# Optimization experiments

Hardware: AMD Instinct MI355X
Metric: run time of the kernel (lower is better)

The kernel has to match this reference:

```python
import jax, jax.numpy as jnp
import numpy as np

N = 100000
E = 1600000
D = 128      # input_dim == hidden_dim
C = 40       # output_dim
L = 3        # num_layers
EPS = 1e-12  # F.normalize eps


def setup_inputs() -> dict:
    key = jax.random.key(0)
    ks = jax.random.split(key, 8)
    x = jax.random.normal(ks[0], (N, D), dtype=jnp.float32)
    edge_index = jax.random.randint(ks[1], (2, E), 0, N, dtype=jnp.int64)
    s = 1.0 / np.sqrt(D)
    # SAGEConv: lin_l (neighbor path, with bias), lin_r (root path, no bias)
    Wl = jax.random.uniform(ks[2], (L, D, D), jnp.float32, -s, s)
    bl = jax.random.uniform(ks[3], (L, D), jnp.float32, -s, s)
    Wr = jax.random.uniform(ks[4], (L, D, D), jnp.float32, -s, s)
    Wlin = jax.random.uniform(ks[5], (C, D), jnp.float32, -s, s)
    blin = jax.random.uniform(ks[6], (C,), jnp.float32, -s, s)
    return {"x": x, "edge_index": edge_index, "Wl": Wl, "bl": bl,
            "Wr": Wr, "Wlin": Wlin, "blin": blin}


def reference(x, edge_index, Wl, bl, Wr, Wlin, blin):
    src, dst = edge_index[0], edge_index[1]
    # in-degree counts for mean aggregation (computed once, reused per layer)
    cnt = jax.ops.segment_sum(jnp.ones((E,), jnp.float32), dst, num_segments=N)
    inv_cnt = (1.0 / jnp.maximum(cnt, 1.0))[:, None]  # [N,1]
    z = x
    for i in range(L):
        msg = z[src]  # gather [E, D]
        agg = jax.ops.segment_sum(msg, dst, num_segments=N) * inv_cnt  # mean [N, D]
        out = agg @ Wl[i].T + bl[i] + z @ Wr[i].T
        # SAGEConv normalize=True: L2 normalize per node
        nrm = jnp.linalg.norm(out, axis=-1, keepdims=True)
        out = out / jnp.maximum(nrm, EPS)
        z = jax.nn.relu(out)  # dropout p=0 -> identity
    return z @ Wlin.T + blin  # [N, C]
```

## Files before the change

### kernel.cpp

```cpp
#include <hip/hip_runtime.h>


typedef __bf16 bf16x8 __attribute__((ext_vector_type(8)));
typedef float  f32x4  __attribute__((ext_vector_type(4)));

#define MFMA16(a, b, c) __builtin_amdgcn_mfma_f32_16x16x32_bf16((a), (b), (c), 0, 0, 0)

__device__ __forceinline__ unsigned rne_bf16(float f) {
  unsigned u = __float_as_uint(f);
  unsigned r = u + 0x7FFFu + ((u >> 16) & 1u);
  return r >> 16;
}

__device__ __forceinline__ float bf_lo(unsigned u) { return __uint_as_float(u << 16); }
__device__ __forceinline__ float bf_hi(unsigned u) { return __uint_as_float(u & 0xFFFF0000u); }

__device__ __forceinline__ void gload_lds16(const void* g, void* l) {
  __builtin_amdgcn_global_load_lds(
      (const __attribute__((address_space(1))) unsigned int*)g,
      (__attribute__((address_space(3))) unsigned int*)l, 16, 0, 0);
}

__global__ __launch_bounds__(256) void prep_k(
    const float* __restrict__ x, const float* __restrict__ Wl,
    const float* __restrict__ Wr, const float* __restrict__ Wlin,
    uint2* __restrict__ planeA, unsigned short* __restrict__ wfrag,
    unsigned short* __restrict__ wlf, int* __restrict__ gcur,
    int cap, int n4) {
  const int b = blockIdx.x;
  const int tid = threadIdx.x;
  if (b == 0) {
    if (tid < 128) gcur[tid] = tid * cap;
    return;
  }
  if (b <= 96) {
    int id = (b - 1) * 256 + tid;
    int l = id & 63;
    int c = (id >> 6) & 7;
    int t = (id >> 9) & 7;
    int p = (id >> 12) & 1;
    int layer = id >> 13;
    int col = t * 16 + (l & 15);
    int kbase = c * 32 + (l >> 4) * 8;
    unsigned short* dst = wfrag + (size_t)layer * 65536 +
                          ((((size_t)p * 8 + t) * 8 + c) * 64 + l) * 8;
#pragma unroll
    for (int j = 0; j < 8; ++j) {
      int k = kbase + j;
      float w = (k < 128) ? Wl[layer * 16384 + col * 128 + k]
                          : Wr[layer * 16384 + col * 128 + (k - 128)];
      unsigned h = rne_bf16(w);
      unsigned o;
      if (p == 0) o = h;
      else o = rne_bf16(w - __uint_as_float(h << 16));
      dst[j] = (unsigned short)o;
    }
    return;
  }
  if (b == 97) {
    for (int id = tid; id < 3 * 4 * 64; id += 256) {
      int l = id & 63;
      int c = (id >> 6) & 3;
      int t = id >> 8;
      int col = t * 16 + (l & 15);
      int kbase = c * 32 + (l >> 4) * 8;
      unsigned short* dst = wlf + (size_t)id * 8;
#pragma unroll
      for (int j = 0; j < 8; ++j) {
        float w = (col < 40) ? Wlin[col * 128 + kbase + j] : 0.f;
        dst[j] = (unsigned short)rne_bf16(w);
      }
    }
    return;
  }
  int i = (b - 98) * 256 + tid;
  if (i >= n4) return;
  float4 f = ((const float4*)x)[i];
  uint2 o;
  o.x = rne_bf16(f.x) | (rne_bf16(f.y) << 16);
  o.y = rne_bf16(f.z) | (rne_bf16(f.w) << 16);
  planeA[i] = o;
}


__global__ __launch_bounds__(256) void bucketA_k(
    const int* __restrict__ src, const int* __restrict__ dst,
    int* __restrict__ gcur, unsigned* __restrict__ coarse, int E, int nc) {
  __shared__ int hist[128];
  __shared__ int sd[128];
  __shared__ int lpos[128];
  __shared__ int gbase[128];
  __shared__ unsigned stage[2048];
  __shared__ unsigned char sbuck[2048];

  const int tid = threadIdx.x;
  const int e0 = blockIdx.x * 2048;

  if (tid < 128) hist[tid] = 0;
  __syncthreads();

  int bv[8], pk[8];
#pragma unroll
  for (int j = 0; j < 8; ++j) {
    int e = e0 + j * 256 + tid;
    bv[j] = -1;
    if (e < E) {
      int s = src[e], d = dst[e];
      bv[j] = d >> 10;
      pk[j] = s | ((d & 1023) << 17);
      atomicAdd(&hist[bv[j]], 1);
    }
  }
  __syncthreads();

  if (tid < 128) sd[tid] = hist[tid];
  __syncthreads();
  for (int off = 1; off < 128; off <<= 1) {
    int t = 0;
    if (tid < 128 && tid >= off) t = sd[tid - off];
    __syncthreads();
    if (tid < 128) sd[tid] += t;
    __syncthreads();
  }
  if (tid < 128) {
    int excl = sd[tid] - hist[tid];
    lpos[tid] = excl;
    gbase[tid] = (tid < nc && hist[tid] > 0) ? atomicAdd(&gcur[tid], hist[tid]) : 0;
  }
  __syncthreads();

#pragma unroll
  for (int j = 0; j < 8; ++j) {
    if (bv[j] >= 0) {
      int slot = atomicAdd(&lpos[bv[j]], 1);
      stage[slot] = (unsigned)pk[j];
      sbuck[slot] = (unsigned char)bv[j];
    }
  }
  __syncthreads();

  const int total = sd[127];
  for (int i = tid; i < total; i += 256) {
    int b = sbuck[i];
    int excl = sd[b] - hist[b];
    coarse[gbase[b] + (i - excl)] = stage[i];
  }
}

__global__ __launch_bounds__(256) void bucketB_k(
    const int* __restrict__ gcur, const unsigned* __restrict__ coarse, int cap,
    int* __restrict__ esrc, int* __restrict__ offsets,
    float* __restrict__ inv_cnt, int n, int nc) {
  __shared__ int hcnt[1024];
  __shared__ int cur[1024];
  __shared__ int sd[256];
  __shared__ int sh_gdst;

  const int tid = threadIdx.x;
  const int b = blockIdx.x;
  const int base = b * 1024;
  const int nn = (n - base < 1024) ? (n - base) : 1024;
  const int wbeg = b * cap;
  const int wend = gcur[b];

  if (tid < 128) {
    int v = (tid < nc) ? (gcur[tid] - tid * cap) : 0;
    sd[tid] = v;
  }
  __syncthreads();
  for (int off = 1; off < 128; off <<= 1) {
    int u = 0;
    if (tid < 128 && tid >= off) u = sd[tid - off];
    __syncthreads();
    if (tid < 128) sd[tid] += u;
    __syncthreads();
  }
  if (tid == b) sh_gdst = sd[tid] - (wend - wbeg);
  for (int j = tid; j < 1024; j += 256) hcnt[j] = 0;
  __syncthreads();
  const int gdst = sh_gdst;

  for (int idx = wbeg + tid; idx < wend; idx += 256)
    atomicAdd(&hcnt[coarse[idx] >> 17], 1);
  __syncthreads();

  int b0 = hcnt[tid * 4], b1 = hcnt[tid * 4 + 1];
  int b2 = hcnt[tid * 4 + 2], b3 = hcnt[tid * 4 + 3];
  int tot = b0 + b1 + b2 + b3;
  sd[tid] = tot;
  __syncthreads();
  for (int off = 1; off < 256; off <<= 1) {
    int u = (tid >= off) ? sd[tid - off] : 0;
    __syncthreads();
    sd[tid] += u;
    __syncthreads();
  }
  int excl = gdst + sd[tid] - tot;
  cur[tid * 4]     = excl;
  cur[tid * 4 + 1] = excl + b0;
  cur[tid * 4 + 2] = excl + b0 + b1;
  cur[tid * 4 + 3] = excl + b0 + b1 + b2;
  __syncthreads();

  for (int j = tid; j < nn; j += 256) {
    offsets[base + j] = cur[j];
    int c = hcnt[j] > 1 ? hcnt[j] : 1;
    inv_cnt[base + j] = 1.0f / (float)c;
  }
  if (tid == 0 && base + nn >= n) offsets[n] = gdst + (wend - wbeg);
  __syncthreads();

  for (int idx = wbeg + tid; idx < wend; idx += 256) {
    unsigned p = coarse[idx];
    int pos = atomicAdd(&cur[p >> 17], 1);
    esrc[pos] = (int)(p & 0x1FFFFu);
  }
}

__global__ void aggregate_k(const unsigned short* __restrict__ zb,
                            const int* __restrict__ offsets,
                            const int* __restrict__ esrc,
                            const float* __restrict__ inv_cnt,
                            unsigned short* __restrict__ aggh, int n) {
  int node = (blockIdx.x * 256 + threadIdx.x) >> 4;
  int l16 = threadIdx.x & 15;
  if (node >= n) return;
  int beg = offsets[node], end = offsets[node + 1];
  float a0 = 0.f, a1 = 0.f, a2 = 0.f, a3 = 0.f;
  float a4 = 0.f, a5 = 0.f, a6 = 0.f, a7 = 0.f;
  int t = beg;
  for (; t + 4 <= end; t += 4) {
    int s0 = esrc[t], s1 = esrc[t + 1], s2 = esrc[t + 2], s3 = esrc[t + 3];
    uint4 d0 = *(const uint4*)(zb + (size_t)s0 * 128 + l16 * 8);
    uint4 d1 = *(const uint4*)(zb + (size_t)s1 * 128 + l16 * 8);
    uint4 d2 = *(const uint4*)(zb + (size_t)s2 * 128 + l16 * 8);
    uint4 d3 = *(const uint4*)(zb + (size_t)s3 * 128 + l16 * 8);
    a0 += bf_lo(d0.x); a1 += bf_hi(d0.x); a2 += bf_lo(d0.y); a3 += bf_hi(d0.y);
    a4 += bf_lo(d0.z); a5 += bf_hi(d0.z); a6 += bf_lo(d0.w); a7 += bf_hi(d0.w);
    a0 += bf_lo(d1.x); a1 += bf_hi(d1.x); a2 += bf_lo(d1.y); a3 += bf_hi(d1.y);
    a4 += bf_lo(d1.z); a5 += bf_hi(d1.z); a6 += bf_lo(d1.w); a7 += bf_hi(d1.w);
    a0 += bf_lo(d2.x); a1 += bf_hi(d2.x); a2 += bf_lo(d2.y); a3 += bf_hi(d2.y);
    a4 += bf_lo(d2.z); a5 += bf_hi(d2.z); a6 += bf_lo(d2.w); a7 += bf_hi(d2.w);
    a0 += bf_lo(d3.x); a1 += bf_hi(d3.x); a2 += bf_lo(d3.y); a3 += bf_hi(d3.y);
    a4 += bf_lo(d3.z); a5 += bf_hi(d3.z); a6 += bf_lo(d3.w); a7 += bf_hi(d3.w);
  }
  for (; t + 2 <= end; t += 2) {
    int s0 = esrc[t], s1 = esrc[t + 1];
    uint4 d0 = *(const uint4*)(zb + (size_t)s0 * 128 + l16 * 8);
    uint4 d1 = *(const uint4*)(zb + (size_t)s1 * 128 + l16 * 8);
    a0 += bf_lo(d0.x); a1 += bf_hi(d0.x); a2 += bf_lo(d0.y); a3 += bf_hi(d0.y);
    a4 += bf_lo(d0.z); a5 += bf_hi(d0.z); a6 += bf_lo(d0.w); a7 += bf_hi(d0.w);
    a0 += bf_lo(d1.x); a1 += bf_hi(d1.x); a2 += bf_lo(d1.y); a3 += bf_hi(d1.y);
    a4 += bf_lo(d1.z); a5 += bf_hi(d1.z); a6 += bf_lo(d1.w); a7 += bf_hi(d1.w);
  }
  if (t < end) {
    int s0 = esrc[t];
    uint4 d0 = *(const uint4*)(zb + (size_t)s0 * 128 + l16 * 8);
    a0 += bf_lo(d0.x); a1 += bf_hi(d0.x); a2 += bf_lo(d0.y); a3 += bf_hi(d0.y);
    a4 += bf_lo(d0.z); a5 += bf_hi(d0.z); a6 += bf_lo(d0.w); a7 += bf_hi(d0.w);
  }
  float ic = inv_cnt[node];
  uint4 hv;
  hv.x = rne_bf16(a0 * ic) | (rne_bf16(a1 * ic) << 16);
  hv.y = rne_bf16(a2 * ic) | (rne_bf16(a3 * ic) << 16);
  hv.z = rne_bf16(a4 * ic) | (rne_bf16(a5 * ic) << 16);
  hv.w = rne_bf16(a6 * ic) | (rne_bf16(a7 * ic) << 16);
  *(uint4*)(aggh + (size_t)node * 128 + l16 * 8) = hv;
}

template <bool FUSE>
__global__ __launch_bounds__(256) void sage_layer_mfma_k(
    const unsigned short* __restrict__ zb, const unsigned short* __restrict__ aggh,
    const unsigned short* __restrict__ wf, const float* __restrict__ bl,
    unsigned short* __restrict__ out_bf,
    const unsigned short* __restrict__ wlf, const float* __restrict__ blin,
    float* __restrict__ fout, int n, int ntiles) {
  __shared__ unsigned short Ah_s[32 * 256];
  __shared__ unsigned short Zt_s[FUSE ? 32 * 128 : 8];
  __shared__ float psum[2][4][16];

  const int lane = threadIdx.x & 63;
  const int wv = threadIdx.x >> 6;
  const int g = lane >> 4;
  const int rl = lane & 15;

  const bf16x8* wfv = (const bf16x8*)wf;
  const int t0 = wv * 2, t1 = wv * 2 + 1;
  bf16x8 Bh0[8], Bh1[8], Bl0[8], Bl1[8];
#pragma unroll
  for (int c = 0; c < 8; ++c) {
    Bh0[c] = wfv[((0 * 8 + t0) * 8 + c) * 64 + lane];
    Bh1[c] = wfv[((0 * 8 + t1) * 8 + c) * 64 + lane];
    Bl0[c] = wfv[((1 * 8 + t0) * 8 + c) * 64 + lane];
    Bl1[c] = wfv[((1 * 8 + t1) * 8 + c) * 64 + lane];
  }
  const float b0 = bl[t0 * 16 + rl];
  const float b1 = bl[t1 * 16 + rl];

  char* pAh = (char*)Ah_s;
  char* pZt = (char*)Zt_s;
  const bf16x8* wlfv = (const bf16x8*)wlf;

  const int rsub = lane >> 5;
  const int hlf = (lane >> 4) & 1;
  const int b16 = lane & 15;

  for (int tile = blockIdx.x; tile < ntiles; tile += gridDim.x) {
    const int v0 = tile * 32;

#pragma unroll
    for (int q = 0; q < 4; ++q) {
      int wq = wv * 4 + q;
      int r = wq * 2 + rsub;
      int v = v0 + r; v = (v < n) ? v : (n - 1);
      int sblk = b16 ^ (r & 7);
      const unsigned short* srcp =
          (hlf ? zb : aggh) + (size_t)v * 128 + sblk * 8;
      gload_lds16(srcp, pAh + wq * 1024);
    }
    __syncthreads();

#pragma unroll
    for (int s = 0; s < 2; ++s) {
      f32x4 a0 = {0.f, 0.f, 0.f, 0.f};
      f32x4 a1 = {0.f, 0.f, 0.f, 0.f};
      const int rowH = (s * 16 + rl) * 512;
      const int swz = (rl & 7) << 4;
#pragma unroll
      for (int c = 0; c < 8; ++c) {
        int offH = (rowH + c * 64 + g * 16) ^ swz;
        bf16x8 ah = *(const bf16x8*)(pAh + offH);
        a0 = MFMA16(ah, Bh0[c], a0); a1 = MFMA16(ah, Bh1[c], a1);
        a0 = MFMA16(ah, Bl0[c], a0); a1 = MFMA16(ah, Bl1[c], a1);
      }
      float pr[4];
#pragma unroll
      for (int j = 0; j < 4; ++j) {
        a0[j] += b0; a1[j] += b1;
        pr[j] = a0[j] * a0[j] + a1[j] * a1[j];
      }
#pragma unroll
      for (int m = 1; m < 16; m <<= 1) {
#pragma unroll
        for (int j = 0; j < 4; ++j) pr[j] += __shfl_xor(pr[j], m);
      }
      if (rl == 0) {
#pragma unroll
        for (int j = 0; j < 4; ++j) psum[s][wv][g * 4 + j] = pr[j];
      }
      __syncthreads();
#pragma unroll
      for (int j = 0; j < 4; ++j) {
        int row16 = g * 4 + j;
        float tot = psum[s][0][row16] + psum[s][1][row16] +
                    psum[s][2][row16] + psum[s][3][row16];
        float inv = 1.0f / fmaxf(sqrtf(tot), 1e-12f);
        int v = v0 + s * 16 + row16;
        float o0 = fmaxf(a0[j] * inv, 0.f);
        float o1 = fmaxf(a1[j] * inv, 0.f);
        unsigned short q0 = (unsigned short)rne_bf16(o0);
        unsigned short q1 = (unsigned short)rne_bf16(o1);
        if (!FUSE) {
          if (v < n) {
            out_bf[(size_t)v * 128 + t0 * 16 + rl] = q0;
            out_bf[(size_t)v * 128 + t1 * 16 + rl] = q1;
          }
        } else {
          int rloc = s * 16 + row16;
          int sw = (rloc & 7) << 4;
          *(unsigned short*)(pZt + ((rloc * 256 + (t0 * 16 + rl) * 2) ^ sw)) = q0;
          *(unsigned short*)(pZt + ((rloc * 256 + (t1 * 16 + rl) * 2) ^ sw)) = q1;
        }
      }
    }

    if (FUSE) {
      __syncthreads();
      for (int job = wv; job < 6; job += 4) {
        int s = job / 3, t = job % 3;
        f32x4 acc = {0.f, 0.f, 0.f, 0.f};
        const int rowz = s * 16 + rl;
        const int swzz = (rowz & 7) << 4;
#pragma unroll
        for (int c = 0; c < 4; ++c) {
          bf16x8 a = *(const bf16x8*)(pZt + ((rowz * 256 + c * 64 + g * 16) ^ swzz));
          bf16x8 bw = wlfv[(t * 4 + c) * 64 + lane];
          acc = MFMA16(a, bw, acc);
        }
        int col = t * 16 + rl;
        if (col < 40) {
          float bb = blin[col];
#pragma unroll
          for (int j = 0; j < 4; ++j) {
            int v = v0 + s * 16 + g * 4 + j;
            if (v < n) fout[(size_t)v * 40 + col] = acc[j] + bb;
          }
        }
      }
    }
    __syncthreads();
  }
}


extern "C" void kernel_launch(void* const* d_in, const int* in_sizes, int n_in,
                              void* d_out, int out_size, void* d_ws, size_t ws_size,
                              hipStream_t stream) {
  const float* x    = (const float*)d_in[0];
  const int*   ei   = (const int*)d_in[1];
  const float* Wl   = (const float*)d_in[2];
  const float* bl   = (const float*)d_in[3];
  const float* Wr   = (const float*)d_in[4];
  const float* Wlin = (const float*)d_in[5];
  const float* blin = (const float*)d_in[6];

  const int N = in_sizes[0] / 128;
  const int E = in_sizes[1] / 2;
  const int D = 128;
  const int NC = (N + 1023) >> 10;
  const int cap = (E + NC - 1) / NC + 4096;

  const int* src = ei;
  const int* dstp = ei + E;

  unsigned short* planeA = (unsigned short*)d_ws;
  unsigned short* planeB = planeA + (size_t)N * D;
  unsigned short* aggh   = planeB + (size_t)N * D;
  float* inv_cnt = (float*)(aggh + (size_t)N * D);
  unsigned short* wlf = (unsigned short*)(inv_cnt + N);
  unsigned short* Wfrag = wlf + 6144;
  int*   offsets = (int*)(Wfrag + 3 * 65536);
  int*   esrc    = offsets + N + 1;
  unsigned* coarse = (unsigned*)(esrc + E);
  int*   gcur    = (int*)(coarse + (size_t)NC * cap);

  const int n4 = N * 32;
  prep_k<<<98 + (n4 + 255) / 256, 256, 0, stream>>>(
      x, Wl, Wr, Wlin, (uint2*)planeA, Wfrag, wlf, gcur, cap, n4);

  bucketA_k<<<(E + 2047) / 2048, 256, 0, stream>>>(src, dstp, gcur, coarse, E, NC);
  bucketB_k<<<NC, 256, 0, stream>>>(gcur, coarse, cap, esrc, offsets, inv_cnt, N, NC);

  const int aggGrid = (N * 16 + 255) / 256;
  const int ntiles = (N + 31) / 32;
  const int sageGrid = 1024;

  aggregate_k<<<aggGrid, 256, 0, stream>>>(planeA, offsets, esrc, inv_cnt, aggh, N);
  sage_layer_mfma_k<false><<<sageGrid, 256, 0, stream>>>(
      planeA, aggh, Wfrag + 0 * 65536, bl + 0 * D, planeB, wlf, blin, nullptr, N, ntiles);
  aggregate_k<<<aggGrid, 256, 0, stream>>>(planeB, offsets, esrc, inv_cnt, aggh, N);
  sage_layer_mfma_k<false><<<sageGrid, 256, 0, stream>>>(
      planeB, aggh, Wfrag + 1 * 65536, bl + 1 * D, planeA, wlf, blin, nullptr, N, ntiles);
  aggregate_k<<<aggGrid, 256, 0, stream>>>(planeA, offsets, esrc, inv_cnt, aggh, N);
  sage_layer_mfma_k<true><<<sageGrid, 256, 0, stream>>>(
      planeA, aggh, Wfrag + 2 * 65536, bl + 2 * D, nullptr, wlf, blin,
      (float*)d_out, N, ntiles);
}
```

Measured before the change: 352.5 us.

## Double-buffer SAGE layer tiles in LDS and merge per-subtile norm reductions

The SAGE layer kernel now prefetches the next tile's aggregate and root features into a second LDS buffer with async global-to-LDS loads while the current tile is computed. Both 16-row subtiles are accumulated together before one shared norm reduction, which cuts the number of barriers per tile. The persistent grid shrinks from 1024 to 768 blocks to account for the larger LDS footprint. The aim is to hide global load latency behind MFMA work. The cost is more LDS per block, which may lower occupancy, and barriers that may force the prefetch to finish early.

```diff
diff --git a/kernel.cpp b/kernel.cpp
--- a/kernel.cpp
+++ b/kernel.cpp
@@ -275,9 +275,9 @@
     unsigned short* __restrict__ out_bf,
     const unsigned short* __restrict__ wlf, const float* __restrict__ blin,
     float* __restrict__ fout, int n, int ntiles) {
-  __shared__ unsigned short Ah_s[32 * 256];
+  __shared__ unsigned short Ah_s[2][32 * 256];
   __shared__ unsigned short Zt_s[FUSE ? 32 * 128 : 8];
-  __shared__ float psum[2][4][16];
+  __shared__ float psum[2][2][4][16];
 
   const int lane = threadIdx.x & 63;
   const int wv = threadIdx.x >> 6;
@@ -297,7 +297,6 @@
   const float b0 = bl[t0 * 16 + rl];
   const float b1 = bl[t1 * 16 + rl];
 
-  char* pAh = (char*)Ah_s;
   char* pZt = (char*)Zt_s;
   const bf16x8* wlfv = (const bf16x8*)wlf;
 
@@ -305,59 +304,101 @@
   const int hlf = (lane >> 4) & 1;
   const int b16 = lane & 15;
 
-  for (int tile = blockIdx.x; tile < ntiles; tile += gridDim.x) {
+  int tile = blockIdx.x;
+  if (tile >= ntiles) return;
+
+  {
     const int v0 = tile * 32;
-
 #pragma unroll
     for (int q = 0; q < 4; ++q) {
       int wq = wv * 4 + q;
       int r = wq * 2 + rsub;
       int v = v0 + r; v = (v < n) ? v : (n - 1);
       int sblk = b16 ^ (r & 7);
-      const unsigned short* srcp =
-          (hlf ? zb : aggh) + (size_t)v * 128 + sblk * 8;
-      gload_lds16(srcp, pAh + wq * 1024);
+      gload_lds16((hlf ? zb : aggh) + (size_t)v * 128 + sblk * 8,
+                  (char*)Ah_s[0] + wq * 1024);
+    }
+  }
+  __syncthreads();
+
+  int cur = 0, par = 0;
+  while (tile < ntiles) {
+    const int next = tile + gridDim.x;
+    if (next < ntiles) {
+      const int v0n = next * 32;
+#pragma unroll
+      for (int q = 0; q < 4; ++q) {
+        int wq = wv * 4 + q;
+        int r = wq * 2 + rsub;
+        int v = v0n + r; v = (v < n) ? v : (n - 1);
+        int sblk = b16 ^ (r & 7);
+        gload_lds16((hlf ? zb : aggh) + (size_t)v * 128 + sblk * 8,
+                    (char*)Ah_s[cur ^ 1] + wq * 1024);
+      }
+    }
+
+    const int v0 = tile * 32;
+    char* pAh = (char*)Ah_s[cur];
+
+    f32x4 a00 = {0.f,0.f,0.f,0.f}, a10 = {0.f,0.f,0.f,0.f};
+    f32x4 a01 = {0.f,0.f,0.f,0.f}, a11 = {0.f,0.f,0.f,0.f};
+    {
+      const int swz = (rl & 7) << 4;
+      const int row0 = rl * 512;
+      const int row1 = (16 + rl) * 512;
+#pragma unroll
+      for (int c = 0; c < 8; ++c) {
+        int o0 = (row0 + c * 64 + g * 16) ^ swz;
+        int o1 = (row1 + c * 64 + g * 16) ^ swz;
+        bf16x8 ah0 = *(const bf16x8*)(pAh + o0);
+        bf16x8 ah1 = *(const bf16x8*)(pAh + o1);
+        a00 = MFMA16(ah0, Bh0[c], a00); a10 = MFMA16(ah0, Bh1[c], a10);
+        a00 = MFMA16(ah0, Bl0[c], a00); a10 = MFMA16(ah0, Bl1[c], a10);
+        a01 = MFMA16(ah1, Bh0[c], a01); a11 = MFMA16(ah1, Bh1[c], a11);
+        a01 = MFMA16(ah1, Bl0[c], a01); a11 = MFMA16(ah1, Bl1[c], a11);
+      }
+    }
+
+    {
+      float pr0[4], pr1[4];
+#pragma unroll
+      for (int j = 0; j < 4; ++j) {
+        a00[j] += b0; a10[j] += b1;
+        a01[j] += b0; a11[j] += b1;
+        pr0[j] = a00[j]*a00[j] + a10[j]*a10[j];
+        pr1[j] = a01[j]*a01[j] + a11[j]*a11[j];
+      }
+#pragma unroll
+      for (int m = 1; m < 16; m <<= 1) {
+#pragma unroll
+        for (int j = 0; j < 4; ++j) {
+          pr0[j] += __shfl_xor(pr0[j], m);
+          pr1[j] += __shfl_xor(pr1[j], m);
+        }
+      }
+      if (rl == 0) {
+#pragma unroll
+        for (int j = 0; j < 4; ++j) {
+          psum[par][0][wv][g * 4 + j] = pr0[j];
+          psum[par][1][wv][g * 4 + j] = pr1[j];
+        }
+      }
     }
     __syncthreads();
 
 #pragma unroll
     for (int s = 0; s < 2; ++s) {
-      f32x4 a0 = {0.f, 0.f, 0.f, 0.f};
-      f32x4 a1 = {0.f, 0.f, 0.f, 0.f};
-      const int rowH = (s * 16 + rl) * 512;
-      const int swz = (rl & 7) << 4;
-#pragma unroll
-      for (int c = 0; c < 8; ++c) {
-        int offH = (rowH + c * 64 + g * 16) ^ swz;
-        bf16x8 ah = *(const bf16x8*)(pAh + offH);
-        a0 = MFMA16(ah, Bh0[c], a0); a1 = MFMA16(ah, Bh1[c], a1);
-        a0 = MFMA16(ah, Bl0[c], a0); a1 = MFMA16(ah, Bl1[c], a1);
-      }
-      float pr[4];
-#pragma unroll
-      for (int j = 0; j < 4; ++j) {
-        a0[j] += b0; a1[j] += b1;
-        pr[j] = a0[j] * a0[j] + a1[j] * a1[j];
-      }
-#pragma unroll
-      for (int m = 1; m < 16; m <<= 1) {
-#pragma unroll
-        for (int j = 0; j < 4; ++j) pr[j] += __shfl_xor(pr[j], m);
-      }
-      if (rl == 0) {
-#pragma unroll
-        for (int j = 0; j < 4; ++j) psum[s][wv][g * 4 + j] = pr[j];
-      }
-      __syncthreads();
+      f32x4& A0 = s ? a01 : a00;
+      f32x4& A1 = s ? a11 : a10;
 #pragma unroll
       for (int j = 0; j < 4; ++j) {
         int row16 = g * 4 + j;
-        float tot = psum[s][0][row16] + psum[s][1][row16] +
-                    psum[s][2][row16] + psum[s][3][row16];
+        float tot = psum[par][s][0][row16] + psum[par][s][1][row16] +
+                    psum[par][s][2][row16] + psum[par][s][3][row16];
         float inv = 1.0f / fmaxf(sqrtf(tot), 1e-12f);
         int v = v0 + s * 16 + row16;
-        float o0 = fmaxf(a0[j] * inv, 0.f);
-        float o1 = fmaxf(a1[j] * inv, 0.f);
+        float o0 = fmaxf(A0[j] * inv, 0.f);
+        float o1 = fmaxf(A1[j] * inv, 0.f);
         unsigned short q0 = (unsigned short)rne_bf16(o0);
         unsigned short q1 = (unsigned short)rne_bf16(o1);
         if (!FUSE) {
@@ -397,8 +438,10 @@
           }
         }
       }
-    }
-    __syncthreads();
+      __syncthreads();
+    }
+
+    tile = next; cur ^= 1; par ^= 1;
   }
 }
 
@@ -443,7 +486,7 @@
 
   const int aggGrid = (N * 16 + 255) / 256;
   const int ntiles = (N + 31) / 32;
-  const int sageGrid = 1024;
+  const int sageGrid = 768;
 
   aggregate_k<<<aggGrid, 256, 0, stream>>>(planeA, offsets, esrc, inv_cnt, aggh, N);
   sage_layer_mfma_k<false><<<sageGrid, 256, 0, stream>>>(
```

After: 366.1 us. 3.9% more time.
